# Optimization experiments

Hardware: AMD Instinct MI355X
Metric: run time of the kernel (lower is better)

The kernel has to match this reference:

```python
import jax, jax.numpy as jnp
import numpy as np

D_MODEL = 1024
H = 16
D_HEAD = D_MODEL // H


def setup_inputs() -> dict:
    key = jax.random.key(0)
    ks = jax.random.split(key, 9)
    B, S = 2, 2048
    x = jax.random.normal(ks[0], (B, S, D_MODEL), dtype=jnp.float32)
    s = 1.0 / np.sqrt(D_HEAD)
    # per-head Q/K/V linears, stacked: W[h, out, in], b[h, out] (torch Linear: y = x W^T + b)
    Wq = jax.random.normal(ks[1], (H, D_HEAD, D_HEAD), dtype=jnp.float32) * s
    bq = jax.random.normal(ks[2], (H, D_HEAD), dtype=jnp.float32) * 0.01
    Wk = jax.random.normal(ks[3], (H, D_HEAD, D_HEAD), dtype=jnp.float32) * s
    bk = jax.random.normal(ks[4], (H, D_HEAD), dtype=jnp.float32) * 0.01
    Wv = jax.random.normal(ks[5], (H, D_HEAD, D_HEAD), dtype=jnp.float32) * s
    bv = jax.random.normal(ks[6], (H, D_HEAD), dtype=jnp.float32) * 0.01
    Wo = jax.random.normal(ks[7], (D_MODEL, D_MODEL), dtype=jnp.float32) / np.sqrt(D_MODEL)
    bo = jax.random.normal(ks[8], (D_MODEL,), dtype=jnp.float32) * 0.01
    return {"x": x, "Wq": Wq, "bq": bq, "Wk": Wk, "bk": bk,
            "Wv": Wv, "bv": bv, "Wo": Wo, "bo": bo}


def reference(x, Wq, bq, Wk, bk, Wv, bv, Wo, bo):
    B, S, D = x.shape
    xh = x.reshape(B, S, H, D_HEAD)  # split along feature dim, head-major
    q = jnp.einsum('bshi,hoi->bsho', xh, Wq) + bq
    k = jnp.einsum('bshi,hoi->bsho', xh, Wk) + bk
    v = jnp.einsum('bshi,hoi->bsho', xh, Wv) + bv
    scale = 1.0 / jnp.sqrt(jnp.asarray(D_HEAD, dtype=x.dtype))  # source scales by sqrt(d_model//h)
    scores = jnp.einsum('bqhd,bkhd->bhqk', q, k) * scale
    causal = jnp.tril(jnp.ones((S, S), dtype=bool))
    scores = jnp.where(causal, scores, -jnp.inf)
    attn = jax.nn.softmax(scores, axis=-1)
    out = jnp.einsum('bhqk,bkhd->bqhd', attn, v).reshape(B, S, D)
    return out @ Wo.T + bo
```

## Files before the change

kernel.cpp:

```cpp
#include <hip/hip_runtime.h>
#include <cstddef>

#define Bc 2
#define Sc 2048
#define Dc 1024
#define Hc 16
#define QSC 0.18033688011112042f

typedef short short8 __attribute__((ext_vector_type(8)));
typedef float floatx4 __attribute__((ext_vector_type(4)));
typedef unsigned short ushort_t;

#if __has_builtin(__builtin_amdgcn_exp2f)
#define EXP2F(x) __builtin_amdgcn_exp2f(x)
#else
#define EXP2F(x) exp2f(x)
#endif

__device__ __forceinline__ unsigned pack2bf(float a, float b) {
    unsigned ua = __float_as_uint(a) + 0x8000u;
    unsigned ub = __float_as_uint(b) + 0x8000u;
    return __builtin_amdgcn_perm(ub, ua, 0x07060302u);
}
__device__ __forceinline__ ushort_t f2bf(float f) {
    return (ushort_t)((__float_as_uint(f) + 0x8000u) >> 16);
}

__global__ __launch_bounds__(256) void wcvt_kernel(
    const float* __restrict__ Wo, const float* __restrict__ Wq,
    const float* __restrict__ Wk, const float* __restrict__ Wv,
    ushort_t* __restrict__ WoB, ushort_t* __restrict__ Wqkvb)
{
    int idx = (blockIdx.x * 256 + threadIdx.x) * 8;
    const float* src; ushort_t* dst;
    if (idx < 1048576) { src = Wo + idx; dst = WoB + idx; }
    else {
        int r = idx - 1048576;
        int w = r >> 16, off = r & 65535;
        src = (w == 0 ? Wq : (w == 1 ? Wk : Wv)) + off;
        dst = Wqkvb + r;
    }
    float4 a = *(const float4*)src;
    float4 c = *(const float4*)(src + 4);
    uint4 o;
    o.x = pack2bf(a.x, a.y); o.y = pack2bf(a.z, a.w);
    o.z = pack2bf(c.x, c.y); o.w = pack2bf(c.z, c.w);
    *(uint4*)dst = o;
}

__global__ __launch_bounds__(256) void qkv_kernel(
    const float* __restrict__ x, const ushort_t* __restrict__ Wqkvb,
    const float* __restrict__ bq, const float* __restrict__ bk, const float* __restrict__ bv,
    ushort_t* __restrict__ Qb, ushort_t* __restrict__ Kf, ushort_t* __restrict__ Vf)
{
    const int blk = blockIdx.x;
    const int st = blk & 31, h = (blk >> 5) & 15, b = blk >> 9;
    const int bh = b * Hc + h, s0 = st * 64;
    const int tid = threadIdx.x, wid = tid >> 6, lane = tid & 63;
    const int lr = lane & 15, quad = lane >> 4;

    __shared__ ushort_t Xs[64 * 72];
    __shared__ ushort_t Wsh[3 * 64 * 72];

    {
        int row = tid >> 2, cg = tid & 3;
        const float* xp = x + ((size_t)(b * Sc + s0 + row)) * Dc + h * 64 + cg * 16;
        float4 v0 = *(const float4*)xp;
        float4 v1 = *(const float4*)(xp + 4);
        float4 v2 = *(const float4*)(xp + 8);
        float4 v3 = *(const float4*)(xp + 12);
        uint4 p0, p1;
        p0.x = pack2bf(v0.x, v0.y); p0.y = pack2bf(v0.z, v0.w);
        p0.z = pack2bf(v1.x, v1.y); p0.w = pack2bf(v1.z, v1.w);
        p1.x = pack2bf(v2.x, v2.y); p1.y = pack2bf(v2.z, v2.w);
        p1.z = pack2bf(v3.x, v3.y); p1.w = pack2bf(v3.z, v3.w);
        *(uint4*)(Xs + row * 72 + cg * 16) = p0;
        *(uint4*)(Xs + row * 72 + cg * 16 + 8) = p1;
    }
    {
        const ushort_t* Wg = Wqkvb + (size_t)h * 4096;
#pragma unroll
        for (int s = 0; s < 6; ++s) {
            int c = tid + s * 256;
            int w = c >> 9, rem = c & 511, row = rem >> 3, part = rem & 7;
            *(short8*)(Wsh + (w * 64 + row) * 72 + part * 8) =
                *(const short8*)(Wg + (size_t)w * 65536 + row * 64 + part * 8);
        }
    }
    __syncthreads();

    short8 af0 = *(const short8*)(Xs + (wid * 16 + lr) * 72 + quad * 8);
    short8 af1 = *(const short8*)(Xs + (wid * 16 + lr) * 72 + 32 + quad * 8);

    const float* bias3[3] = {bq + h * 64, bk + h * 64, bv + h * 64};
    const int row = tid >> 2, cg = tid & 3;

#pragma unroll
    for (int w = 0; w < 3; ++w) {
        ushort_t* Ot = Wsh + w * 64 * 72;
        short8 bf0[4], bf1[4];
#pragma unroll
        for (int n = 0; n < 4; ++n) {
            const ushort_t* wrow = Ot + (n * 16 + lr) * 72;
            bf0[n] = *(const short8*)(wrow + quad * 8);
            bf1[n] = *(const short8*)(wrow + 32 + quad * 8);
        }
        floatx4 acc[4];
#pragma unroll
        for (int n = 0; n < 4; ++n) {
            floatx4 z = {0.f, 0.f, 0.f, 0.f};
            acc[n] = __builtin_amdgcn_mfma_f32_16x16x32_bf16(af0, bf0[n], z, 0, 0, 0);
            acc[n] = __builtin_amdgcn_mfma_f32_16x16x32_bf16(af1, bf1[n], acc[n], 0, 0, 0);
        }
        __syncthreads();
        if (w < 2) {
#pragma unroll
            for (int n = 0; n < 4; ++n) {
                float bias = bias3[w][n * 16 + lr];
#pragma unroll
                for (int r = 0; r < 4; ++r) {
                    float val = acc[n][r] + bias;
                    if (w == 0) val *= QSC;
                    Ot[(wid * 16 + quad * 4 + r) * 72 + n * 16 + lr] = f2bf(val);
                }
            }
        } else {
#pragma unroll
            for (int n = 0; n < 4; ++n) {
                float bias = bias3[2][n * 16 + lr];
                uint2 pw;
                pw.x = pack2bf(acc[n][0] + bias, acc[n][1] + bias);
                pw.y = pack2bf(acc[n][2] + bias, acc[n][3] + bias);
                *(uint2*)(Ot + (n * 16 + lr) * 72 + wid * 16 + quad * 4) = pw;
            }
        }
        __syncthreads();
        if (w == 0) {
            const ushort_t* srcp = Ot + row * 72 + cg * 16;
            uint4 d0 = *(const uint4*)srcp;
            uint4 d1 = *(const uint4*)(srcp + 8);
            ushort_t* dst = Qb + ((size_t)bh * Sc + s0 + row) * 64 + cg * 16;
            *(uint4*)dst = d0;
            *(uint4*)(dst + 8) = d1;
        } else if (w == 1) {
            uint4 d0 = *(const uint4*)(Ot + (4 * lr + wid) * 72 + 8 * quad);
            uint4 d1 = *(const uint4*)(Ot + (4 * lr + wid) * 72 + 32 + 8 * quad);
            ushort_t* dstb = Kf + ((size_t)(bh * 32 + st)) * 4096 + wid * 1024 + lane * 8;
            *(uint4*)dstb = d0;
            *(uint4*)(dstb + 512) = d1;
        } else {
            uint4 d0 = *(const uint4*)(Ot + (wid * 16 + lr) * 72 + 16 * quad);
            uint4 d1 = *(const uint4*)(Ot + (wid * 16 + lr) * 72 + 16 * quad + 8);
            ushort_t* dstb = Vf + ((size_t)(bh * 32 + st)) * 4096 + wid * 1024 + lane * 8;
            *(uint4*)dstb = d0;
            *(uint4*)(dstb + 512) = d1;
        }
    }
}

__global__ __launch_bounds__(256, 3) void attn_kernel(
    const ushort_t* __restrict__ Qg, const ushort_t* __restrict__ Kfg,
    const ushort_t* __restrict__ Vfg, ushort_t* __restrict__ Actx)
{
    const int blk = blockIdx.x;
    const int x = blk & 7;
    const int bh = ((blk >> 3) & 3) * 8 + x;
    const int fbase = (blk >> 5) & 7;
    const int f = (blk < 256) ? fbase : 15 - fbase;
    const int b = bh >> 4, h = bh & 15;
    const int qta = 31 - f, qtb = f;
    const int s0a = qta * 64, s0b = qtb * 64;
    const int tid = threadIdx.x, wid = tid >> 6, lane = tid & 63;
    const int lr = lane & 15, quad = lane >> 4;

    const ushort_t* Kfb = Kfg + (size_t)bh * 32 * 4096 + lane * 8;
    const ushort_t* Vfb = Vfg + (size_t)bh * 32 * 4096 + lane * 8;

    const ushort_t* QrA = Qg + ((size_t)bh * Sc + s0a + wid * 16 + lr) * 64;
    const ushort_t* QrB = Qg + ((size_t)bh * Sc + s0b + wid * 16 + lr) * 64;
    short8 qfa0 = *(const short8*)(QrA + quad * 8);
    short8 qfa1 = *(const short8*)(QrA + 32 + quad * 8);
    short8 qfb0 = *(const short8*)(QrB + quad * 8);
    short8 qfb1 = *(const short8*)(QrB + 32 + quad * 8);

    floatx4 oA[4], oB[4];
    float lA = 0.f, lB = 0.f;
#pragma unroll
    for (int n = 0; n < 4; ++n) { oA[n] = floatx4{0,0,0,0}; oB[n] = floatx4{0,0,0,0}; }

    for (int kt = 0; kt <= qta; ++kt) {
        const bool hasB = (kt <= qtb);
        const ushort_t* Kt = Kfb + (size_t)kt * 4096;
        const ushort_t* Vt = Vfb + (size_t)kt * 4096;

        short8 kf[4][2], vf[4][2];
#pragma unroll
        for (int kg = 0; kg < 4; ++kg) {
            kf[kg][0] = *(const short8*)(Kt + kg * 1024);
            kf[kg][1] = *(const short8*)(Kt + kg * 1024 + 512);
        }
#pragma unroll
        for (int n = 0; n < 4; ++n) {
            vf[n][0] = *(const short8*)(Vt + n * 1024);
            vf[n][1] = *(const short8*)(Vt + n * 1024 + 512);
        }

        floatx4 sA[4], sB[4];
        __builtin_amdgcn_s_setprio(1);
#pragma unroll
        for (int kg = 0; kg < 4; ++kg) {
            floatx4 z = {0.f, 0.f, 0.f, 0.f};
            floatx4 t0 = __builtin_amdgcn_mfma_f32_16x16x32_bf16(kf[kg][0], qfa0, z, 0, 0, 0);
            sA[kg] = __builtin_amdgcn_mfma_f32_16x16x32_bf16(kf[kg][1], qfa1, t0, 0, 0, 0);
        }
        if (hasB) {
#pragma unroll
            for (int kg = 0; kg < 4; ++kg) {
                floatx4 z = {0.f, 0.f, 0.f, 0.f};
                floatx4 t0 = __builtin_amdgcn_mfma_f32_16x16x32_bf16(kf[kg][0], qfb0, z, 0, 0, 0);
                sB[kg] = __builtin_amdgcn_mfma_f32_16x16x32_bf16(kf[kg][1], qfb1, t0, 0, 0, 0);
            }
        }
        __builtin_amdgcn_s_setprio(0);

        const int qrow = wid * 16 + lr;
        if (kt == qta) {
#pragma unroll
            for (int kg = 0; kg < 4; ++kg)
#pragma unroll
                for (int r = 0; r < 4; ++r)
                    if (16 * quad + 4 * r + kg > qrow) sA[kg][r] = -1e30f;
        }
        if (hasB && kt == qtb) {
#pragma unroll
            for (int kg = 0; kg < 4; ++kg)
#pragma unroll
                for (int r = 0; r < 4; ++r)
                    if (16 * quad + 4 * r + kg > qrow) sB[kg][r] = -1e30f;
        }

        {
            float e[4][4];
#pragma unroll
            for (int kg = 0; kg < 4; ++kg)
#pragma unroll
                for (int r = 0; r < 4; ++r) e[kg][r] = EXP2F(sA[kg][r]);
#pragma unroll
            for (int kg = 0; kg < 4; ++kg)
                lA += (e[kg][0] + e[kg][1]) + (e[kg][2] + e[kg][3]);
            union { uint4 u; short8 s; } p0, p1;
            p0.u.x = pack2bf(e[0][0], e[1][0]); p0.u.y = pack2bf(e[2][0], e[3][0]);
            p0.u.z = pack2bf(e[0][1], e[1][1]); p0.u.w = pack2bf(e[2][1], e[3][1]);
            p1.u.x = pack2bf(e[0][2], e[1][2]); p1.u.y = pack2bf(e[2][2], e[3][2]);
            p1.u.z = pack2bf(e[0][3], e[1][3]); p1.u.w = pack2bf(e[2][3], e[3][3]);
            __builtin_amdgcn_s_setprio(1);
#pragma unroll
            for (int n = 0; n < 4; ++n) {
                oA[n] = __builtin_amdgcn_mfma_f32_16x16x32_bf16(p0.s, vf[n][0], oA[n], 0, 0, 0);
                oA[n] = __builtin_amdgcn_mfma_f32_16x16x32_bf16(p1.s, vf[n][1], oA[n], 0, 0, 0);
            }
            __builtin_amdgcn_s_setprio(0);
        }
        if (hasB) {
            float e[4][4];
#pragma unroll
            for (int kg = 0; kg < 4; ++kg)
#pragma unroll
                for (int r = 0; r < 4; ++r) e[kg][r] = EXP2F(sB[kg][r]);
#pragma unroll
            for (int kg = 0; kg < 4; ++kg)
                lB += (e[kg][0] + e[kg][1]) + (e[kg][2] + e[kg][3]);
            union { uint4 u; short8 s; } p0, p1;
            p0.u.x = pack2bf(e[0][0], e[1][0]); p0.u.y = pack2bf(e[2][0], e[3][0]);
            p0.u.z = pack2bf(e[0][1], e[1][1]); p0.u.w = pack2bf(e[2][1], e[3][1]);
            p1.u.x = pack2bf(e[0][2], e[1][2]); p1.u.y = pack2bf(e[2][2], e[3][2]);
            p1.u.z = pack2bf(e[0][3], e[1][3]); p1.u.w = pack2bf(e[2][3], e[3][3]);
            __builtin_amdgcn_s_setprio(1);
#pragma unroll
            for (int n = 0; n < 4; ++n) {
                oB[n] = __builtin_amdgcn_mfma_f32_16x16x32_bf16(p0.s, vf[n][0], oB[n], 0, 0, 0);
                oB[n] = __builtin_amdgcn_mfma_f32_16x16x32_bf16(p1.s, vf[n][1], oB[n], 0, 0, 0);
            }
            __builtin_amdgcn_s_setprio(0);
        }
    }

    lA += __shfl_xor(lA, 16, 64); lA += __shfl_xor(lA, 32, 64);
    lB += __shfl_xor(lB, 16, 64); lB += __shfl_xor(lB, 32, 64);
    float invA = 1.f / lA, invB = 1.f / lB;
#pragma unroll
    for (int r = 0; r < 4; ++r) {
        float iA = __shfl(invA, 4 * quad + r, 64);
        float iB = __shfl(invB, 4 * quad + r, 64);
        int rowA = s0a + wid * 16 + quad * 4 + r;
        int rowB = s0b + wid * 16 + quad * 4 + r;
        ushort_t* dA = Actx + ((size_t)(b * Sc + rowA)) * Dc + h * 64 + lr;
        ushort_t* dB = Actx + ((size_t)(b * Sc + rowB)) * Dc + h * 64 + lr;
#pragma unroll
        for (int n = 0; n < 4; ++n) {
            dA[n * 16] = f2bf(oA[n][r] * iA);
            dB[n * 16] = f2bf(oB[n][r] * iB);
        }
    }
}

__global__ __launch_bounds__(256, 2) void proj_kernel(
    const ushort_t* __restrict__ Ab, const ushort_t* __restrict__ Wb,
    const float* __restrict__ bo, float* __restrict__ out)
{
    const int bn = blockIdx.x & 15, bm = blockIdx.x >> 4;
    const int tid = threadIdx.x, wid = tid >> 6, lane = tid & 63;
    const int lr = lane & 15, quad = lane >> 4;
    const int wm = wid * 32;

    __shared__ ushort_t As[128 * 40];
    __shared__ ushort_t Bs[64 * 40];

    floatx4 acc[2][4];
#pragma unroll
    for (int i = 0; i < 2; ++i)
#pragma unroll
        for (int n = 0; n < 4; ++n) acc[i][n] = floatx4{0.f, 0.f, 0.f, 0.f};

    const ushort_t* Ag = Ab + (size_t)bm * 128 * 1024;
    const ushort_t* Wg = Wb + (size_t)bn * 64 * 1024;

    const int ar0 = tid >> 2, ap0 = tid & 3;
    const int ar1 = ar0 + 64;

    short8 a0 = *(const short8*)(Ag + (size_t)ar0 * 1024 + ap0 * 8);
    short8 a1 = *(const short8*)(Ag + (size_t)ar1 * 1024 + ap0 * 8);
    short8 b0 = *(const short8*)(Wg + (size_t)ar0 * 1024 + ap0 * 8);
    *(short8*)(As + ar0 * 40 + ap0 * 8) = a0;
    *(short8*)(As + ar1 * 40 + ap0 * 8) = a1;
    *(short8*)(Bs + ar0 * 40 + ap0 * 8) = b0;
    __syncthreads();

    for (int k0 = 0; k0 < 1024; k0 += 32) {
        short8 fa0 = *(const short8*)(As + (wm + lr) * 40 + quad * 8);
        short8 fa1 = *(const short8*)(As + (wm + 16 + lr) * 40 + quad * 8);
        short8 fb[4];
#pragma unroll
        for (int n = 0; n < 4; ++n)
            fb[n] = *(const short8*)(Bs + (n * 16 + lr) * 40 + quad * 8);

        if (k0 < 992) {
            int k1 = k0 + 32;
            a0 = *(const short8*)(Ag + (size_t)ar0 * 1024 + k1 + ap0 * 8);
            a1 = *(const short8*)(Ag + (size_t)ar1 * 1024 + k1 + ap0 * 8);
            b0 = *(const short8*)(Wg + (size_t)ar0 * 1024 + k1 + ap0 * 8);
        }
#pragma unroll
        for (int n = 0; n < 4; ++n) {
            acc[0][n] = __builtin_amdgcn_mfma_f32_16x16x32_bf16(fa0, fb[n], acc[0][n], 0, 0, 0);
            acc[1][n] = __builtin_amdgcn_mfma_f32_16x16x32_bf16(fa1, fb[n], acc[1][n], 0, 0, 0);
        }
        __syncthreads();
        if (k0 < 992) {
            *(short8*)(As + ar0 * 40 + ap0 * 8) = a0;
            *(short8*)(As + ar1 * 40 + ap0 * 8) = a1;
            *(short8*)(Bs + ar0 * 40 + ap0 * 8) = b0;
            __syncthreads();
        }
    }

#pragma unroll
    for (int i = 0; i < 2; ++i) {
        int mrow = bm * 128 + wm + i * 16 + quad * 4;
#pragma unroll
        for (int n = 0; n < 4; ++n) {
            int col = bn * 64 + n * 16 + lr;
            float bias = bo[col];
#pragma unroll
            for (int r = 0; r < 4; ++r)
                out[(size_t)(mrow + r) * 1024 + col] = acc[i][n][r] + bias;
        }
    }
}

extern "C" void kernel_launch(void* const* d_in, const int* in_sizes, int n_in,
                              void* d_out, int out_size, void* d_ws, size_t ws_size,
                              hipStream_t stream)
{
    (void)in_sizes; (void)n_in; (void)out_size; (void)ws_size;
    const float* x  = (const float*)d_in[0];
    const float* Wq = (const float*)d_in[1];
    const float* bq = (const float*)d_in[2];
    const float* Wk = (const float*)d_in[3];
    const float* bk = (const float*)d_in[4];
    const float* Wv = (const float*)d_in[5];
    const float* bv = (const float*)d_in[6];
    const float* Wo = (const float*)d_in[7];
    const float* bo = (const float*)d_in[8];
    float* out = (float*)d_out;

    const size_t N4 = (size_t)Bc * Hc * Sc * 64;
    ushort_t* base  = (ushort_t*)d_ws;
    ushort_t* Qb    = base;
    ushort_t* Kf    = base + N4;
    ushort_t* Vf    = base + 2 * N4;
    ushort_t* Actx  = base + 3 * N4;
    ushort_t* WoB   = base + 4 * N4;
    ushort_t* Wqkvb = base + 4 * N4 + 1048576;

    wcvt_kernel<<<dim3(608), dim3(256), 0, stream>>>(Wo, Wq, Wk, Wv, WoB, Wqkvb);
    qkv_kernel<<<dim3(Bc * Hc * (Sc / 64)), dim3(256), 0, stream>>>(
        x, Wqkvb, bq, bk, bv, Qb, Kf, Vf);
    attn_kernel<<<dim3(512), dim3(256), 0, stream>>>(Qb, Kf, Vf, Actx);
    proj_kernel<<<dim3(32 * 16), dim3(256), 0, stream>>>(Actx, WoB, bo, out);
}
```

Before: 143.3 us.

## Fuse weight bf16 conversion into QKV and projection kernels, widen proj K-tile

Removes the separate weight-conversion kernel and converts the fp32 Wq/Wk/Wv and Wo weights to bf16 on the fly while staging them into shared memory inside the QKV and output-projection kernels. The projection kernel's K step is doubled from 32 to 64, with larger padded LDS tiles, so it runs fewer sync iterations. This saves one kernel launch and the workspace round trip for converted weights. In exchange, Wo is read as fp32 (twice the bytes) by every row block and converted again in each block.

```diff
diff --git a/kernel.cpp b/kernel.cpp
--- a/kernel.cpp
+++ b/kernel.cpp
@@ -26,30 +26,9 @@
     return (ushort_t)((__float_as_uint(f) + 0x8000u) >> 16);
 }
 
-__global__ __launch_bounds__(256) void wcvt_kernel(
-    const float* __restrict__ Wo, const float* __restrict__ Wq,
-    const float* __restrict__ Wk, const float* __restrict__ Wv,
-    ushort_t* __restrict__ WoB, ushort_t* __restrict__ Wqkvb)
-{
-    int idx = (blockIdx.x * 256 + threadIdx.x) * 8;
-    const float* src; ushort_t* dst;
-    if (idx < 1048576) { src = Wo + idx; dst = WoB + idx; }
-    else {
-        int r = idx - 1048576;
-        int w = r >> 16, off = r & 65535;
-        src = (w == 0 ? Wq : (w == 1 ? Wk : Wv)) + off;
-        dst = Wqkvb + r;
-    }
-    float4 a = *(const float4*)src;
-    float4 c = *(const float4*)(src + 4);
-    uint4 o;
-    o.x = pack2bf(a.x, a.y); o.y = pack2bf(a.z, a.w);
-    o.z = pack2bf(c.x, c.y); o.w = pack2bf(c.z, c.w);
-    *(uint4*)dst = o;
-}
-
 __global__ __launch_bounds__(256) void qkv_kernel(
-    const float* __restrict__ x, const ushort_t* __restrict__ Wqkvb,
+    const float* __restrict__ x,
+    const float* __restrict__ Wq, const float* __restrict__ Wk, const float* __restrict__ Wv,
     const float* __restrict__ bq, const float* __restrict__ bk, const float* __restrict__ bv,
     ushort_t* __restrict__ Qb, ushort_t* __restrict__ Kf, ushort_t* __restrict__ Vf)
 {
@@ -78,13 +57,18 @@
         *(uint4*)(Xs + row * 72 + cg * 16 + 8) = p1;
     }
     {
-        const ushort_t* Wg = Wqkvb + (size_t)h * 4096;
 #pragma unroll
         for (int s = 0; s < 6; ++s) {
             int c = tid + s * 256;
             int w = c >> 9, rem = c & 511, row = rem >> 3, part = rem & 7;
-            *(short8*)(Wsh + (w * 64 + row) * 72 + part * 8) =
-                *(const short8*)(Wg + (size_t)w * 65536 + row * 64 + part * 8);
+            const float* wp = (w == 0 ? Wq : (w == 1 ? Wk : Wv))
+                              + (size_t)h * 4096 + row * 64 + part * 8;
+            float4 v0 = *(const float4*)wp;
+            float4 v1 = *(const float4*)(wp + 4);
+            uint4 o;
+            o.x = pack2bf(v0.x, v0.y); o.y = pack2bf(v0.z, v0.w);
+            o.z = pack2bf(v1.x, v1.y); o.w = pack2bf(v1.z, v1.w);
+            *(uint4*)(Wsh + (w * 64 + row) * 72 + part * 8) = o;
         }
     }
     __syncthreads();
@@ -305,7 +289,7 @@
 }
 
 __global__ __launch_bounds__(256, 2) void proj_kernel(
-    const ushort_t* __restrict__ Ab, const ushort_t* __restrict__ Wb,
+    const ushort_t* __restrict__ Ab, const float* __restrict__ WoF,
     const float* __restrict__ bo, float* __restrict__ out)
 {
     const int bn = blockIdx.x & 15, bm = blockIdx.x >> 4;
@@ -313,8 +297,8 @@
     const int lr = lane & 15, quad = lane >> 4;
     const int wm = wid * 32;
 
-    __shared__ ushort_t As[128 * 40];
-    __shared__ ushort_t Bs[64 * 40];
+    __shared__ ushort_t As[128 * 72];
+    __shared__ ushort_t Bs[64 * 72];
 
     floatx4 acc[2][4];
 #pragma unroll
@@ -323,43 +307,76 @@
         for (int n = 0; n < 4; ++n) acc[i][n] = floatx4{0.f, 0.f, 0.f, 0.f};
 
     const ushort_t* Ag = Ab + (size_t)bm * 128 * 1024;
-    const ushort_t* Wg = Wb + (size_t)bn * 64 * 1024;
-
-    const int ar0 = tid >> 2, ap0 = tid & 3;
-    const int ar1 = ar0 + 64;
-
-    short8 a0 = *(const short8*)(Ag + (size_t)ar0 * 1024 + ap0 * 8);
-    short8 a1 = *(const short8*)(Ag + (size_t)ar1 * 1024 + ap0 * 8);
-    short8 b0 = *(const short8*)(Wg + (size_t)ar0 * 1024 + ap0 * 8);
-    *(short8*)(As + ar0 * 40 + ap0 * 8) = a0;
-    *(short8*)(As + ar1 * 40 + ap0 * 8) = a1;
-    *(short8*)(Bs + ar0 * 40 + ap0 * 8) = b0;
+    const float* Wg = WoF + (size_t)bn * 64 * 1024;
+
+    const int arow = tid >> 1, acol = (tid & 1) * 32;
+    const int brow = tid >> 2, bcol = (tid & 3) * 16;
+
+    short8 a0, a1, a2, a3;
+    float4 b0, b1, b2, b3;
+
+    {
+        const ushort_t* ap = Ag + (size_t)arow * 1024 + acol;
+        a0 = *(const short8*)(ap);      a1 = *(const short8*)(ap + 8);
+        a2 = *(const short8*)(ap + 16); a3 = *(const short8*)(ap + 24);
+        const float* bp = Wg + (size_t)brow * 1024 + bcol;
+        b0 = *(const float4*)(bp);      b1 = *(const float4*)(bp + 4);
+        b2 = *(const float4*)(bp + 8);  b3 = *(const float4*)(bp + 12);
+        ushort_t* aw = As + arow * 72 + acol;
+        *(short8*)(aw) = a0;      *(short8*)(aw + 8) = a1;
+        *(short8*)(aw + 16) = a2; *(short8*)(aw + 24) = a3;
+        uint4 w0, w1;
+        w0.x = pack2bf(b0.x, b0.y); w0.y = pack2bf(b0.z, b0.w);
+        w0.z = pack2bf(b1.x, b1.y); w0.w = pack2bf(b1.z, b1.w);
+        w1.x = pack2bf(b2.x, b2.y); w1.y = pack2bf(b2.z, b2.w);
+        w1.z = pack2bf(b3.x, b3.y); w1.w = pack2bf(b3.z, b3.w);
+        ushort_t* bw = Bs + brow * 72 + bcol;
+        *(uint4*)(bw) = w0;
+        *(uint4*)(bw + 8) = w1;
+    }
     __syncthreads();
 
-    for (int k0 = 0; k0 < 1024; k0 += 32) {
-        short8 fa0 = *(const short8*)(As + (wm + lr) * 40 + quad * 8);
-        short8 fa1 = *(const short8*)(As + (wm + 16 + lr) * 40 + quad * 8);
-        short8 fb[4];
-#pragma unroll
-        for (int n = 0; n < 4; ++n)
-            fb[n] = *(const short8*)(Bs + (n * 16 + lr) * 40 + quad * 8);
-
-        if (k0 < 992) {
-            int k1 = k0 + 32;
-            a0 = *(const short8*)(Ag + (size_t)ar0 * 1024 + k1 + ap0 * 8);
-            a1 = *(const short8*)(Ag + (size_t)ar1 * 1024 + k1 + ap0 * 8);
-            b0 = *(const short8*)(Wg + (size_t)ar0 * 1024 + k1 + ap0 * 8);
-        }
-#pragma unroll
-        for (int n = 0; n < 4; ++n) {
-            acc[0][n] = __builtin_amdgcn_mfma_f32_16x16x32_bf16(fa0, fb[n], acc[0][n], 0, 0, 0);
-            acc[1][n] = __builtin_amdgcn_mfma_f32_16x16x32_bf16(fa1, fb[n], acc[1][n], 0, 0, 0);
-        }
+    for (int k0 = 0; k0 < 1024; k0 += 64) {
+        short8 fa0[2], fa1[2], fb[2][4];
+#pragma unroll
+        for (int kh = 0; kh < 2; ++kh) {
+            fa0[kh] = *(const short8*)(As + (wm + lr) * 72 + kh * 32 + quad * 8);
+            fa1[kh] = *(const short8*)(As + (wm + 16 + lr) * 72 + kh * 32 + quad * 8);
+#pragma unroll
+            for (int n = 0; n < 4; ++n)
+                fb[kh][n] = *(const short8*)(Bs + (n * 16 + lr) * 72 + kh * 32 + quad * 8);
+        }
+
+        if (k0 < 960) {
+            int k1 = k0 + 64;
+            const ushort_t* ap = Ag + (size_t)arow * 1024 + k1 + acol;
+            a0 = *(const short8*)(ap);      a1 = *(const short8*)(ap + 8);
+            a2 = *(const short8*)(ap + 16); a3 = *(const short8*)(ap + 24);
+            const float* bp = Wg + (size_t)brow * 1024 + k1 + bcol;
+            b0 = *(const float4*)(bp);      b1 = *(const float4*)(bp + 4);
+            b2 = *(const float4*)(bp + 8);  b3 = *(const float4*)(bp + 12);
+        }
+
+#pragma unroll
+        for (int kh = 0; kh < 2; ++kh)
+#pragma unroll
+            for (int n = 0; n < 4; ++n) {
+                acc[0][n] = __builtin_amdgcn_mfma_f32_16x16x32_bf16(fa0[kh], fb[kh][n], acc[0][n], 0, 0, 0);
+                acc[1][n] = __builtin_amdgcn_mfma_f32_16x16x32_bf16(fa1[kh], fb[kh][n], acc[1][n], 0, 0, 0);
+            }
         __syncthreads();
-        if (k0 < 992) {
-            *(short8*)(As + ar0 * 40 + ap0 * 8) = a0;
-            *(short8*)(As + ar1 * 40 + ap0 * 8) = a1;
-            *(short8*)(Bs + ar0 * 40 + ap0 * 8) = b0;
+        if (k0 < 960) {
+            ushort_t* aw = As + arow * 72 + acol;
+            *(short8*)(aw) = a0;      *(short8*)(aw + 8) = a1;
+            *(short8*)(aw + 16) = a2; *(short8*)(aw + 24) = a3;
+            uint4 w0, w1;
+            w0.x = pack2bf(b0.x, b0.y); w0.y = pack2bf(b0.z, b0.w);
+            w0.z = pack2bf(b1.x, b1.y); w0.w = pack2bf(b1.z, b1.w);
+            w1.x = pack2bf(b2.x, b2.y); w1.y = pack2bf(b2.z, b2.w);
+            w1.z = pack2bf(b3.x, b3.y); w1.w = pack2bf(b3.z, b3.w);
+            ushort_t* bw = Bs + brow * 72 + bcol;
+            *(uint4*)(bw) = w0;
+            *(uint4*)(bw + 8) = w1;
             __syncthreads();
         }
     }
@@ -400,12 +417,9 @@
     ushort_t* Kf    = base + N4;
     ushort_t* Vf    = base + 2 * N4;
     ushort_t* Actx  = base + 3 * N4;
-    ushort_t* WoB   = base + 4 * N4;
-    ushort_t* Wqkvb = base + 4 * N4 + 1048576;
-
-    wcvt_kernel<<<dim3(608), dim3(256), 0, stream>>>(Wo, Wq, Wk, Wv, WoB, Wqkvb);
+
     qkv_kernel<<<dim3(Bc * Hc * (Sc / 64)), dim3(256), 0, stream>>>(
-        x, Wqkvb, bq, bk, bv, Qb, Kf, Vf);
+        x, Wq, Wk, Wv, bq, bk, bv, Qb, Kf, Vf);
     attn_kernel<<<dim3(512), dim3(256), 0, stream>>>(Qb, Kf, Vf, Actx);
-    proj_kernel<<<dim3(32 * 16), dim3(256), 0, stream>>>(Actx, WoB, bo, out);
-}
+    proj_kernel<<<dim3(32 * 16), dim3(256), 0, stream>>>(Actx, Wo, bo, out);
+}
```

Result: no change. 141.1 us (-1.6%).
